# Kernel optimization log

Hardware: AMD Instinct MI355X
Metric: run time of the kernel (lower is better)

The kernel has to match this reference:

```python
import jax, jax.numpy as jnp
import numpy as np

EPS = 1e-10  # SILogLoss eps


def _onedir(a, valid_a, b, valid_b):
    # Faithful to ChamferDistanceLoss.onedirectional_dist with inf-masking semantics:
    # invalid b entries (inf in torch) are excluded from the min; rows whose min is
    # +inf (invalid a, or no valid b) contribute 0. a,b: [B,Na],[B,Nb].
    d2 = (a[:, :, None] - b[:, None, :]) ** 2            # [B, Na, Nb]
    d2 = jnp.where(valid_b[:, None, :], d2, jnp.inf)
    m = jnp.min(d2, axis=2)                              # [B, Na]
    m = jnp.where(valid_a & jnp.isfinite(m), m, 0.0)
    return m.sum(axis=1)                                 # [B]


def setup_inputs() -> dict:
    key = jax.random.key(0)
    k1, k2, k3, k4 = jax.random.split(key, 4)
    B, H, W, NB = 4, 480, 640, 128
    prediction = jax.random.uniform(k1, (B, 1, H, W), dtype=jnp.float32)
    target = jax.random.uniform(k2, (B, 1, H, W), dtype=jnp.float32)
    bin_edges = jax.random.uniform(k3, (B, NB), dtype=jnp.float32)
    mask = jax.random.bernoulli(k4, 0.95, (B, 1, H, W))  # bool, mostly valid
    return {"prediction": prediction, "target": target, "bin_edges": bin_edges, "mask": mask}


def reference(prediction, target, bin_edges, mask):
    w_silog, w_l2, w_bins = 1.0, 1.0, 1.0  # w_masked = 1.0 -> invalid branch skipped
    B = target.shape[0]
    mflat = mask.reshape(B, -1)                          # [B, H*W] bool
    tflat = target.reshape(B, -1)
    pflat = prediction.reshape(B, -1)

    # --- Chamfer (scale-invariant): normalize by per-image masked max / per-row bin max
    tmax = jnp.max(jnp.where(mflat, tflat, -jnp.inf), axis=1, keepdims=True)   # [B,1]
    bmax = jnp.max(bin_edges, axis=1, keepdims=True)                            # [B,1]
    t_n = jnp.where(mflat, tflat / tmax, 0.0)            # invalid pixels excluded via mask
    b_n = bin_edges / bmax                               # the +inf pad bin contributes 0, omitted
    bvalid = jnp.ones(b_n.shape, dtype=bool)
    chamfer = (_onedir(b_n, bvalid, t_n, mflat) + _onedir(t_n, mflat, b_n, bvalid)).mean()

    # --- masked SILog + L2 (means over valid pixels only)
    m = mflat.astype(prediction.dtype)
    n = m.sum()
    d = jnp.log(pflat + EPS) - jnp.log(tflat + EPS)
    mean_d = (m * d).sum() / n
    mean_d2 = (m * d * d).sum() / n
    silog = 10.0 * jnp.sqrt(mean_d2 - 0.85 * mean_d ** 2)
    l2 = jnp.sqrt((m * (pflat - tflat) ** 2).sum() / n)

    return w_l2 * l2 + w_silog * silog + w_bins * chamfer
```

## Files before the change

### kernel.cpp

```cpp
#include <hip/hip_runtime.h>
#include <math.h>

#define HW_TOT (480*640)
#define NQ (HW_TOT/4)
#define NBATCH 4
#define NB 128
#define NGAP (NB+1)
#define SBX 75
#define EPSV 1e-10f
#define INF_BITS 0x7F800000u

__device__ __forceinline__ int nzbytes(unsigned x) {
  return ((x & 0xFFu) != 0) + ((x & 0xFF00u) != 0) +
         ((x & 0xFF0000u) != 0) + ((x >> 24) != 0);
}

__device__ __forceinline__ void sniff_mask(const void* mask, int tid, int* smode) {
  if (tid < 64) {
    const uint4* m16 = (const uint4*)mask;
    uint4 w = m16[tid];
    int c = nzbytes(w.x) + nzbytes(w.y) + nzbytes(w.z) + nzbytes(w.w);
#pragma unroll
    for (int off = 32; off > 0; off >>= 1) c += __shfl_down(c, off);
    if (tid == 0) *smode = (c >= 768) ? 0 : 1;
  }
}

__device__ __forceinline__ void mask4(const void* mask, int e, int mode, bool v[4]) {
  if (mode == 0) {
    unsigned mw = *(const unsigned*)((const unsigned char*)mask + e);
    v[0] = (mw & 0xFFu) != 0;        v[1] = ((mw >> 8) & 0xFFu) != 0;
    v[2] = ((mw >> 16) & 0xFFu) != 0; v[3] = (mw >> 24) != 0;
  } else {
    int4 mi = *(const int4*)((const int*)mask + e);
    v[0] = mi.x != 0; v[1] = mi.y != 0; v[2] = mi.z != 0; v[3] = mi.w != 0;
  }
}

__global__ __launch_bounds__(256) void k_stats(const float* __restrict__ pred,
                                               const float* __restrict__ targ,
                                               const void* __restrict__ mask,
                                               const float* __restrict__ bins,
                                               float* __restrict__ bn,
                                               float4* __restrict__ pacc,
                                               float* __restrict__ ptmax) {
  const int b = blockIdx.y, bx = blockIdx.x, tid = threadIdx.x;
  __shared__ int smode;
  sniff_mask(mask, tid, &smode);
  __syncthreads();
  const int mode = smode;
  const int base = b * HW_TOT;

  float cnt = 0.f, sd = 0.f, sd2 = 0.f, sl2 = 0.f, tm = 0.f;
#pragma unroll
  for (int k = 0; k < 4; ++k) {
    const int q = bx * 1024 + k * 256 + tid;
    const int e = base + q * 4;
    const float4 t4 = *(const float4*)(targ + e);
    const float4 p4 = *(const float4*)(pred + e);
    bool v[4];
    mask4(mask, e, mode, v);
    const float t[4] = {t4.x, t4.y, t4.z, t4.w};
    const float p[4] = {p4.x, p4.y, p4.z, p4.w};
#pragma unroll
    for (int j = 0; j < 4; ++j) {
      const float m = v[j] ? 1.f : 0.f;
      const float d = logf(p[j] + EPSV) - logf(t[j] + EPSV);
      cnt += m;
      sd  += m * d;
      sd2 += m * d * d;
      const float er = p[j] - t[j];
      sl2 += m * er * er;
      if (v[j]) tm = fmaxf(tm, t[j]);
    }
  }
#pragma unroll
  for (int off = 32; off > 0; off >>= 1) {
    cnt += __shfl_down(cnt, off);
    sd  += __shfl_down(sd,  off);
    sd2 += __shfl_down(sd2, off);
    sl2 += __shfl_down(sl2, off);
    tm   = fmaxf(tm, __shfl_down(tm, off));
  }
  __shared__ float red[4][5];
  const int wave = tid >> 6, lane = tid & 63;
  if (lane == 0) {
    red[wave][0] = cnt; red[wave][1] = sd; red[wave][2] = sd2;
    red[wave][3] = sl2; red[wave][4] = tm;
  }
  __syncthreads();
  if (tid == 0) {
    float C = 0, S = 0, S2 = 0, L = 0, T = 0;
#pragma unroll
    for (int w = 0; w < 4; ++w) {
      C += red[w][0]; S += red[w][1]; S2 += red[w][2]; L += red[w][3];
      T = fmaxf(T, red[w][4]);
    }
    pacc[b * SBX + bx] = make_float4(C, S, S2, L);
    ptmax[b * SBX + bx] = T;
  }

  if (bx == 0) {
    __shared__ float sb[NB];
    __shared__ float sred2[64];
    if (tid < NB) sb[tid] = bins[b * NB + tid];
    __syncthreads();
    if (tid < 64) sred2[tid] = fmaxf(sb[tid], sb[tid + 64]);
    __syncthreads();
    for (int s = 32; s > 0; s >>= 1) {
      if (tid < s) sred2[tid] = fmaxf(sred2[tid], sred2[tid + s]);
      __syncthreads();
    }
    const float bmax = sred2[0];
    __syncthreads();
    if (tid < NB) sb[tid] = bins[b * NB + tid] / bmax;
    __syncthreads();
    for (int k = 2; k <= NB; k <<= 1) {
      for (int jj = k >> 1; jj > 0; jj >>= 1) {
        const int ixj = tid ^ jj;
        if (tid < NB && ixj > tid) {
          const float a = sb[tid], c = sb[ixj];
          const bool up = ((tid & k) == 0);
          if (up ? (a > c) : (a < c)) { sb[tid] = c; sb[ixj] = a; }
        }
        __syncthreads();
      }
    }
    if (tid < NB) bn[b * NB + tid] = sb[tid];
  }
}

__global__ __launch_bounds__(256) void k_chamfer(const float* __restrict__ targ,
                                                 const void* __restrict__ mask,
                                                 const float* __restrict__ bn,
                                                 const float* __restrict__ ptmax,
                                                 float* __restrict__ pcsum,
                                                 unsigned* __restrict__ pgmin,
                                                 unsigned* __restrict__ pgmax,
                                                 int nbx) {
  const int b = blockIdx.y, bx = blockIdx.x, tid = threadIdx.x;
  __shared__ int smode;
  __shared__ float sbn[NB];
  __shared__ unsigned sgmin[NGAP], sgmax[NGAP];
  __shared__ float stmax;

  sniff_mask(mask, tid, &smode);
  if (tid < NB) sbn[tid] = bn[b * NB + tid];
  if (tid < NGAP) { sgmin[tid] = INF_BITS; sgmax[tid] = 0u; }
  if (tid >= 128 && tid < 192) {
    const int l = tid - 128;
    float v = (l < SBX) ? ptmax[b * SBX + l] : 0.f;
    if (l + 64 < SBX) v = fmaxf(v, ptmax[b * SBX + l + 64]);
#pragma unroll
    for (int off = 32; off > 0; off >>= 1) v = fmaxf(v, __shfl_down(v, off));
    if (l == 0) stmax = v;
  }
  __syncthreads();
  const int mode = smode;
  const float tmax = stmax;
  const int base = b * HW_TOT;

  float csum = 0.f;
  for (int q = bx * 256 + tid; q < NQ; q += nbx * 256) {
    const int e = base + q * 4;
    const float4 t4 = *(const float4*)(targ + e);
    bool v[4];
    mask4(mask, e, mode, v);
    const float t[4] = {t4.x, t4.y, t4.z, t4.w};
#pragma unroll
    for (int k = 0; k < 4; ++k) {
      if (v[k]) {
        const float tn = t[k] / tmax;
        int pos = 0;
#pragma unroll
        for (int s = 64; s > 0; s >>= 1) {
          const int np = pos + s;
          if (np <= NB && sbn[np - 1] < tn) pos = np;
        }
        if (sbn[NB - 1] < tn) pos = NB;
        const float c0 = sbn[pos > 0 ? pos - 1 : 0];
        const float c1 = sbn[pos < NB ? pos : NB - 1];
        const float d0 = tn - c0, d1 = tn - c1;
        csum += fminf(d0 * d0, d1 * d1);
        const unsigned tb = __float_as_uint(tn);
        atomicMin(&sgmin[pos], tb);
        atomicMax(&sgmax[pos], tb);
      }
    }
  }
#pragma unroll
  for (int off = 32; off > 0; off >>= 1) csum += __shfl_down(csum, off);
  __shared__ float cred[4];
  const int wave = tid >> 6, lane = tid & 63;
  if (lane == 0) cred[wave] = csum;
  __syncthreads();
  const int slot = b * nbx + bx;
  if (tid == 0) pcsum[slot] = cred[0] + cred[1] + cred[2] + cred[3];
  if (tid < NGAP) {
    pgmin[slot * NGAP + tid] = sgmin[tid];
    pgmax[slot * NGAP + tid] = sgmax[tid];
  }
}

__global__ __launch_bounds__(64) void k_merge(const unsigned* __restrict__ pgmin,
                                              const unsigned* __restrict__ pgmax,
                                              unsigned* __restrict__ mgmin,
                                              unsigned* __restrict__ mgmax,
                                              int nbx) {
  const int g = blockIdx.x, b = blockIdx.y, tid = threadIdx.x;
  unsigned mn = INF_BITS, mx = 0u;
  for (int k = tid; k < nbx; k += 64) {
    mn = min(mn, pgmin[(b * nbx + k) * NGAP + g]);
    mx = max(mx, pgmax[(b * nbx + k) * NGAP + g]);
  }
#pragma unroll
  for (int off = 32; off > 0; off >>= 1) {
    mn = min(mn, (unsigned)__shfl_down((int)mn, off));
    mx = max(mx, (unsigned)__shfl_down((int)mx, off));
  }
  if (tid == 0) { mgmin[b * NGAP + g] = mn; mgmax[b * NGAP + g] = mx; }
}

__global__ __launch_bounds__(512) void k_final(const float* __restrict__ bn,
                                               const float4* __restrict__ pacc,
                                               const float* __restrict__ pcsum,
                                               const unsigned* __restrict__ mgmin,
                                               const unsigned* __restrict__ mgmax,
                                               int nbx,
                                               float* __restrict__ out) {
  const int tid = threadIdx.x;
  __shared__ double wacc[8][4];
  __shared__ unsigned smgmin[NBATCH * NGAP], smgmax[NBATCH * NGAP];
  __shared__ double sc[512];
  __shared__ float sred[512];

  double a0 = 0, a1 = 0, a2 = 0, a3 = 0;
  if (tid < NBATCH * SBX) {
    const float4 p = pacc[tid];
    a0 = p.x; a1 = p.y; a2 = p.z; a3 = p.w;
  }
#pragma unroll
  for (int off = 32; off > 0; off >>= 1) {
    a0 += __shfl_down(a0, off); a1 += __shfl_down(a1, off);
    a2 += __shfl_down(a2, off); a3 += __shfl_down(a3, off);
  }
  if ((tid & 63) == 0) {
    wacc[tid >> 6][0] = a0; wacc[tid >> 6][1] = a1;
    wacc[tid >> 6][2] = a2; wacc[tid >> 6][3] = a3;
  }
  for (int o = tid; o < NBATCH * NGAP; o += 512) {
    smgmin[o] = mgmin[o]; smgmax[o] = mgmax[o];
  }
  sc[tid] = (tid < NBATCH * nbx) ? (double)pcsum[tid] : 0.0;
  __syncthreads();
  for (int s = nbx >> 1; s > 0; s >>= 1) {
    if (tid < NBATCH * nbx && (tid & (nbx - 1)) < s) sc[tid] += sc[tid + s];
    __syncthreads();
  }

  const int b = tid >> 7, j = tid & 127;
  const float bnj = bn[b * NB + j];
  float md = INFINITY;
  for (int g = 0; g < NGAP; ++g) {
    const float gmn = __uint_as_float(smgmin[b * NGAP + g]);
    const float gmx = __uint_as_float(smgmax[b * NGAP + g]);
    const float d = fmaxf(fmaxf(gmn - bnj, bnj - gmx), 0.0f);
    md = fminf(md, d * d);
  }
  sred[tid] = isfinite(md) ? md : 0.0f;
  __syncthreads();
  for (int s = 64; s > 0; s >>= 1) {
    if (j < s) sred[tid] += sred[tid + s];
    __syncthreads();
  }
  if (tid == 0) {
    double n = 0, sdv = 0, sd2v = 0, sl2v = 0;
#pragma unroll
    for (int w = 0; w < 8; ++w) {
      n += wacc[w][0]; sdv += wacc[w][1]; sd2v += wacc[w][2]; sl2v += wacc[w][3];
    }
    const double mean_d = sdv / n, mean_d2 = sd2v / n;
    const double silog = 10.0 * sqrt(mean_d2 - 0.85 * mean_d * mean_d);
    const double l2 = sqrt(sl2v / n);
    double ch = 0.0;
    for (int bb = 0; bb < NBATCH; ++bb)
      ch += sc[bb * nbx] + (double)sred[bb * 128];
    ch /= (double)NBATCH;
    out[0] = (float)(l2 + silog + ch);
  }
}

extern "C" void kernel_launch(void* const* d_in, const int* in_sizes, int n_in,
                              void* d_out, int out_size, void* d_ws, size_t ws_size,
                              hipStream_t stream) {
  const float* pred = (const float*)d_in[0];
  const float* targ = (const float*)d_in[1];
  const float* bins = (const float*)d_in[2];
  const void*  mask = d_in[3];
  float* out = (float*)d_out;

  char* w = (char*)d_ws;
  float*    bn    = (float*)w;
  float4*   pacc  = (float4*)(w + 2048);
  float*    ptmax = (float*)(w + 6848);
  unsigned* mgmin = (unsigned*)(w + 8064);
  unsigned* mgmax = (unsigned*)(w + 10128);
  const size_t hdr = 12288;
  auto need = [&](size_t nb) {
    return hdr + NBATCH * nb * sizeof(float) +
           2 * NBATCH * nb * NGAP * sizeof(unsigned);
  };
  int nbx = 128;
  if (ws_size < need(128)) nbx = (ws_size >= need(16)) ? 16 : 4;
  float*    pcsum = (float*)(w + hdr);
  unsigned* pgmin = (unsigned*)(w + hdr + NBATCH * nbx * sizeof(float));
  unsigned* pgmax = pgmin + NBATCH * (size_t)nbx * NGAP;

  k_stats<<<dim3(SBX, NBATCH), dim3(256), 0, stream>>>(pred, targ, mask, bins,
                                                       bn, pacc, ptmax);
  k_chamfer<<<dim3(nbx, NBATCH), dim3(256), 0, stream>>>(targ, mask, bn, ptmax,
                                                         pcsum, pgmin, pgmax, nbx);
  k_merge<<<dim3(NGAP, NBATCH), dim3(64), 0, stream>>>(pgmin, pgmax,
                                                       mgmin, mgmax, nbx);
  k_final<<<dim3(1), dim3(512), 0, stream>>>(bn, pacc, pcsum, mgmin, mgmax,
                                             nbx, out);
}
```

Measured before the change: 98.76 us.

## Fuse merge and final reduction into chamfer kernel via global atomics and last-block ticket

Chamfer blocks now atomically merge their per-gap min/max directly into global arrays, which k_stats initializes. A completion ticket counter lets the last block perform the final loss reduction. This removes the k_merge and k_final launches and the per-block partial gap buffers, cutting launch overhead and extra global traffic. In exchange it adds global atomics, threadfences and a serial tail on a single 256-thread block.

```diff
diff --git a/kernel.cpp b/kernel.cpp
--- a/kernel.cpp
+++ b/kernel.cpp
@@ -37,13 +37,23 @@
   }
 }
 
+__device__ __forceinline__ unsigned aload_u(const unsigned* p) {
+  return __hip_atomic_load(p, __ATOMIC_RELAXED, __HIP_MEMORY_SCOPE_AGENT);
+}
+__device__ __forceinline__ float aload_f(const float* p) {
+  return __hip_atomic_load(p, __ATOMIC_RELAXED, __HIP_MEMORY_SCOPE_AGENT);
+}
+
 __global__ __launch_bounds__(256) void k_stats(const float* __restrict__ pred,
                                                const float* __restrict__ targ,
                                                const void* __restrict__ mask,
                                                const float* __restrict__ bins,
                                                float* __restrict__ bn,
                                                float4* __restrict__ pacc,
-                                               float* __restrict__ ptmax) {
+                                               float* __restrict__ ptmax,
+                                               unsigned* __restrict__ mgmin,
+                                               unsigned* __restrict__ mgmax,
+                                               unsigned* __restrict__ done) {
   const int b = blockIdx.y, bx = blockIdx.x, tid = threadIdx.x;
   __shared__ int smode;
   sniff_mask(mask, tid, &smode);
@@ -101,6 +111,9 @@
   }
 
   if (bx == 0) {
+    if (tid < NGAP) { mgmin[b * NGAP + tid] = INF_BITS; mgmax[b * NGAP + tid] = 0u; }
+    if (b == 0 && tid == 0) *done = 0u;
+
     __shared__ float sb[NB];
     __shared__ float sred2[64];
     if (tid < NB) sb[tid] = bins[b * NB + tid];
@@ -134,10 +147,13 @@
                                                  const void* __restrict__ mask,
                                                  const float* __restrict__ bn,
                                                  const float* __restrict__ ptmax,
+                                                 const float4* __restrict__ pacc,
                                                  float* __restrict__ pcsum,
-                                                 unsigned* __restrict__ pgmin,
-                                                 unsigned* __restrict__ pgmax,
-                                                 int nbx) {
+                                                 unsigned* __restrict__ mgmin,
+                                                 unsigned* __restrict__ mgmax,
+                                                 unsigned* __restrict__ done,
+                                                 int nbx,
+                                                 float* __restrict__ out) {
   const int b = blockIdx.y, bx = blockIdx.x, tid = threadIdx.x;
   __shared__ int smode;
   __shared__ float sbn[NB];
@@ -195,88 +211,79 @@
   if (lane == 0) cred[wave] = csum;
   __syncthreads();
   const int slot = b * nbx + bx;
-  if (tid == 0) pcsum[slot] = cred[0] + cred[1] + cred[2] + cred[3];
+  if (tid == 0)
+    __hip_atomic_store(&pcsum[slot], cred[0] + cred[1] + cred[2] + cred[3],
+                       __ATOMIC_RELAXED, __HIP_MEMORY_SCOPE_AGENT);
   if (tid < NGAP) {
-    pgmin[slot * NGAP + tid] = sgmin[tid];
-    pgmax[slot * NGAP + tid] = sgmax[tid];
-  }
-}
-
-__global__ __launch_bounds__(64) void k_merge(const unsigned* __restrict__ pgmin,
-                                              const unsigned* __restrict__ pgmax,
-                                              unsigned* __restrict__ mgmin,
-                                              unsigned* __restrict__ mgmax,
-                                              int nbx) {
-  const int g = blockIdx.x, b = blockIdx.y, tid = threadIdx.x;
-  unsigned mn = INF_BITS, mx = 0u;
-  for (int k = tid; k < nbx; k += 64) {
-    mn = min(mn, pgmin[(b * nbx + k) * NGAP + g]);
-    mx = max(mx, pgmax[(b * nbx + k) * NGAP + g]);
-  }
-#pragma unroll
-  for (int off = 32; off > 0; off >>= 1) {
-    mn = min(mn, (unsigned)__shfl_down((int)mn, off));
-    mx = max(mx, (unsigned)__shfl_down((int)mx, off));
-  }
-  if (tid == 0) { mgmin[b * NGAP + g] = mn; mgmax[b * NGAP + g] = mx; }
-}
-
-__global__ __launch_bounds__(512) void k_final(const float* __restrict__ bn,
-                                               const float4* __restrict__ pacc,
-                                               const float* __restrict__ pcsum,
-                                               const unsigned* __restrict__ mgmin,
-                                               const unsigned* __restrict__ mgmax,
-                                               int nbx,
-                                               float* __restrict__ out) {
-  const int tid = threadIdx.x;
-  __shared__ double wacc[8][4];
+    if (sgmin[tid] != INF_BITS) atomicMin(&mgmin[b * NGAP + tid], sgmin[tid]);
+    if (sgmax[tid] != 0u)       atomicMax(&mgmax[b * NGAP + tid], sgmax[tid]);
+  }
+  __syncthreads();
+  __shared__ unsigned sticket;
+  if (tid == 0) {
+    __threadfence();
+    sticket = atomicAdd(done, 1u);
+  }
+  __syncthreads();
+  if (sticket != (unsigned)(nbx * NBATCH - 1)) return;
+
+  __threadfence();
+  __shared__ double wacc[4][4];
   __shared__ unsigned smgmin[NBATCH * NGAP], smgmax[NBATCH * NGAP];
-  __shared__ double sc[512];
-  __shared__ float sred[512];
+  __shared__ double scd[NBATCH * NB];
+  __shared__ float sredf[NBATCH * NB];
 
   double a0 = 0, a1 = 0, a2 = 0, a3 = 0;
-  if (tid < NBATCH * SBX) {
-    const float4 p = pacc[tid];
-    a0 = p.x; a1 = p.y; a2 = p.z; a3 = p.w;
+  for (int i = tid; i < NBATCH * SBX; i += 256) {
+    const float4 p = pacc[i];
+    a0 += p.x; a1 += p.y; a2 += p.z; a3 += p.w;
   }
 #pragma unroll
   for (int off = 32; off > 0; off >>= 1) {
     a0 += __shfl_down(a0, off); a1 += __shfl_down(a1, off);
     a2 += __shfl_down(a2, off); a3 += __shfl_down(a3, off);
   }
-  if ((tid & 63) == 0) {
-    wacc[tid >> 6][0] = a0; wacc[tid >> 6][1] = a1;
-    wacc[tid >> 6][2] = a2; wacc[tid >> 6][3] = a3;
-  }
-  for (int o = tid; o < NBATCH * NGAP; o += 512) {
-    smgmin[o] = mgmin[o]; smgmax[o] = mgmax[o];
-  }
-  sc[tid] = (tid < NBATCH * nbx) ? (double)pcsum[tid] : 0.0;
+  if (lane == 0) {
+    wacc[wave][0] = a0; wacc[wave][1] = a1;
+    wacc[wave][2] = a2; wacc[wave][3] = a3;
+  }
+  for (int o = tid; o < NBATCH * NGAP; o += 256) {
+    smgmin[o] = aload_u(&mgmin[o]);
+    smgmax[o] = aload_u(&mgmax[o]);
+  }
+  for (int o = tid; o < NBATCH * nbx; o += 256) scd[o] = (double)aload_f(&pcsum[o]);
   __syncthreads();
   for (int s = nbx >> 1; s > 0; s >>= 1) {
-    if (tid < NBATCH * nbx && (tid & (nbx - 1)) < s) sc[tid] += sc[tid + s];
-    __syncthreads();
-  }
-
-  const int b = tid >> 7, j = tid & 127;
-  const float bnj = bn[b * NB + j];
-  float md = INFINITY;
-  for (int g = 0; g < NGAP; ++g) {
-    const float gmn = __uint_as_float(smgmin[b * NGAP + g]);
-    const float gmx = __uint_as_float(smgmax[b * NGAP + g]);
-    const float d = fmaxf(fmaxf(gmn - bnj, bnj - gmx), 0.0f);
-    md = fminf(md, d * d);
-  }
-  sred[tid] = isfinite(md) ? md : 0.0f;
+    for (int o = tid; o < NBATCH * s; o += 256) {
+      const int bb = o / s, j = o - bb * s;
+      scd[bb * nbx + j] += scd[bb * nbx + j + s];
+    }
+    __syncthreads();
+  }
+  for (int r = tid; r < NBATCH * NB; r += 256) {
+    const int bb = r >> 7, j = r & 127;
+    const float bnj = bn[bb * NB + j];
+    float md = INFINITY;
+    for (int g = 0; g < NGAP; ++g) {
+      const float gmn = __uint_as_float(smgmin[bb * NGAP + g]);
+      const float gmx = __uint_as_float(smgmax[bb * NGAP + g]);
+      const float d = fmaxf(fmaxf(gmn - bnj, bnj - gmx), 0.0f);
+      md = fminf(md, d * d);
+    }
+    sredf[r] = isfinite(md) ? md : 0.0f;
+  }
   __syncthreads();
   for (int s = 64; s > 0; s >>= 1) {
-    if (j < s) sred[tid] += sred[tid + s];
+    for (int o = tid; o < NBATCH * s; o += 256) {
+      const int bb = o / s, j = o - bb * s;
+      sredf[bb * NB + j] += sredf[bb * NB + j + s];
+    }
     __syncthreads();
   }
   if (tid == 0) {
     double n = 0, sdv = 0, sd2v = 0, sl2v = 0;
 #pragma unroll
-    for (int w = 0; w < 8; ++w) {
+    for (int w = 0; w < 4; ++w) {
       n += wacc[w][0]; sdv += wacc[w][1]; sd2v += wacc[w][2]; sl2v += wacc[w][3];
     }
     const double mean_d = sdv / n, mean_d2 = sd2v / n;
@@ -284,7 +291,7 @@
     const double l2 = sqrt(sl2v / n);
     double ch = 0.0;
     for (int bb = 0; bb < NBATCH; ++bb)
-      ch += sc[bb * nbx] + (double)sred[bb * 128];
+      ch += scd[bb * nbx] + (double)sredf[bb * NB];
     ch /= (double)NBATCH;
     out[0] = (float)(l2 + silog + ch);
   }
@@ -305,23 +312,17 @@
   float*    ptmax = (float*)(w + 6848);
   unsigned* mgmin = (unsigned*)(w + 8064);
   unsigned* mgmax = (unsigned*)(w + 10128);
+  unsigned* done  = (unsigned*)(w + 12192);
   const size_t hdr = 12288;
-  auto need = [&](size_t nb) {
-    return hdr + NBATCH * nb * sizeof(float) +
-           2 * NBATCH * nb * NGAP * sizeof(unsigned);
-  };
   int nbx = 128;
-  if (ws_size < need(128)) nbx = (ws_size >= need(16)) ? 16 : 4;
-  float*    pcsum = (float*)(w + hdr);
-  unsigned* pgmin = (unsigned*)(w + hdr + NBATCH * nbx * sizeof(float));
-  unsigned* pgmax = pgmin + NBATCH * (size_t)nbx * NGAP;
+  if (ws_size < hdr + 128 * NBATCH * sizeof(float)) nbx = 4;
+  float* pcsum = (float*)(w + hdr);
 
   k_stats<<<dim3(SBX, NBATCH), dim3(256), 0, stream>>>(pred, targ, mask, bins,
-                                                       bn, pacc, ptmax);
+                                                       bn, pacc, ptmax,
+                                                       mgmin, mgmax, done);
   k_chamfer<<<dim3(nbx, NBATCH), dim3(256), 0, stream>>>(targ, mask, bn, ptmax,
-                                                         pcsum, pgmin, pgmax, nbx);
-  k_merge<<<dim3(NGAP, NBATCH), dim3(64), 0, stream>>>(pgmin, pgmax,
-                                                       mgmin, mgmax, nbx);
-  k_final<<<dim3(1), dim3(512), 0, stream>>>(bn, pacc, pcsum, mgmin, mgmax,
-                                             nbx, out);
-}
+                                                         pacc, pcsum,
+                                                         mgmin, mgmax, done,
+                                                         nbx, out);
+}
```

Result: slower. 109.7 us (+11.1%).
